# Performance work log

Hardware: AMD Instinct MI355X
Metric: run time of the kernel (lower is better)

The kernel has to match this reference:

```python
import jax, jax.numpy as jnp
from jax import lax
import numpy as np

NHEADS = 8

def _conv_block2d(x, w, b):
    y = lax.conv_general_dilated(x, w, (2, 2), [(1, 1), (1, 1)],
                                 dimension_numbers=('NCHW', 'OIHW', 'NCHW'))
    return jax.nn.gelu(y + b[None, :, None, None])

def _conv_block3d(x, w, b):
    y = lax.conv_general_dilated(x, w, (2, 2, 2), [(1, 1)] * 3,
                                 dimension_numbers=('NCDHW', 'OIDHW', 'NCDHW'))
    return jax.nn.gelu(y + b[None, :, None, None, None])

def _layernorm(x, g, b, eps=1e-5):
    mu = x.mean(-1, keepdims=True)
    var = x.var(-1, keepdims=True)
    return (x - mu) / jnp.sqrt(var + eps) * g + b

def _neighborhood_attn(x, g, bln, qkv_w, qkv_b, proj_w, proj_b, dw=5, hw=7, ww=7):
    # x: [B, C, D, H, W]; 3D neighborhood attention, window (dw,hw,ww), zero-pad + mask
    B, C, D, H, W = x.shape
    h, hd = NHEADS, C // NHEADS
    xt = jnp.transpose(x, (0, 2, 3, 4, 1))               # [B,D,H,W,C]
    y = _layernorm(xt, g, bln)
    qkv = y @ qkv_w + qkv_b                               # [B,D,H,W,3C]
    qkv = qkv.reshape(B, D, H, W, 3, h, hd)
    qkv = jnp.transpose(qkv, (4, 0, 5, 6, 1, 2, 3))       # [3,B,h,hd,D,H,W]
    q, k, v = qkv[0] * (hd ** -0.5), qkv[1], qkv[2]
    pz, py, px = dw // 2, hw // 2, ww // 2
    pad = ((0, 0), (0, 0), (0, 0), (pz, pz), (py, py), (px, px))
    kp, vp = jnp.pad(k, pad), jnp.pad(v, pad)
    valid = jnp.pad(jnp.ones((D, H, W), x.dtype), ((pz, pz), (py, py), (px, px)))
    offs = jnp.stack(jnp.meshgrid(jnp.arange(dw), jnp.arange(hw), jnp.arange(ww), indexing='ij'), -1).reshape(-1, 3)

    def score_step(_, o):
        ks = lax.dynamic_slice(kp, (0, 0, 0, o[0], o[1], o[2]), (B, h, hd, D, H, W))
        m = lax.dynamic_slice(valid, (o[0], o[1], o[2]), (D, H, W))
        return None, ((q * ks).sum(2), m)

    _, (scores, masks) = lax.scan(score_step, None, offs)  # [245,B,h,D,H,W],[245,D,H,W]
    neg = jnp.finfo(scores.dtype).min
    scores = jnp.where(masks[:, None, None] > 0, scores, neg)
    probs = jax.nn.softmax(scores, axis=0)

    def out_step(acc, xs):
        o, p = xs
        vs = lax.dynamic_slice(vp, (0, 0, 0, o[0], o[1], o[2]), (B, h, hd, D, H, W))
        return acc + p[:, :, None] * vs, None

    out0 = jnp.zeros((B, h, hd, D, H, W), x.dtype)
    out, _ = lax.scan(out_step, out0, (offs, probs))
    out = jnp.transpose(out, (0, 3, 4, 5, 1, 2)).reshape(B, D, H, W, C)
    out = out @ proj_w + proj_b
    return x + jnp.transpose(out, (0, 4, 1, 2, 3))

def setup_inputs() -> dict:
    key = jax.random.key(0)
    ks = jax.random.split(key, 16)
    rn = lambda i, shp, s: jax.random.normal(ks[i], shp, jnp.float32) * s
    return {
        'x_2d': rn(0, (1, 8, 256, 512), 1.0),
        'x_3d': rn(1, (1, 5, 24, 256, 512), 1.0),
        'sw0': rn(2, (128, 8, 3, 3), 0.02), 'sb0': jnp.zeros((128,), jnp.float32),
        'sw1': rn(3, (256, 128, 3, 3), 0.02), 'sb1': jnp.zeros((256,), jnp.float32),
        'sw2': rn(4, (512, 256, 3, 3), 0.02), 'sb2': jnp.zeros((512,), jnp.float32),
        'pw0': rn(5, (128, 5, 3, 3, 3), 0.02), 'pb0': jnp.zeros((128,), jnp.float32),
        'pw1': rn(6, (256, 128, 3, 3, 3), 0.02), 'pb1': jnp.zeros((256,), jnp.float32),
        'pw2': rn(7, (512, 256, 3, 3, 3), 0.02), 'pb2': jnp.zeros((512,), jnp.float32),
        'lat_w': rn(8, (512, 512, 1, 1, 1), 0.02), 'lat_b': jnp.zeros((512,), jnp.float32),
        'ln_g': jnp.ones((3, 512), jnp.float32), 'ln_b': jnp.zeros((3, 512), jnp.float32),
        'qkv_w': rn(9, (3, 512, 1536), 0.02), 'qkv_b': jnp.zeros((3, 1536), jnp.float32),
        'proj_w': rn(10, (3, 512, 512), 0.02), 'proj_b': jnp.zeros((3, 512), jnp.float32),
    }

def reference(x_2d, x_3d, sw0, sb0, sw1, sb1, sw2, sb2,
              pw0, pb0, pw1, pb1, pw2, pb2, lat_w, lat_b,
              ln_g, ln_b, qkv_w, qkv_b, proj_w, proj_b):
    s = x_2d
    for w_, b_ in ((sw0, sb0), (sw1, sb1), (sw2, sb2)):
        s = _conv_block2d(s, w_, b_)
    p = x_3d
    for w_, b_ in ((pw0, pb0), (pw1, pb1), (pw2, pb2)):
        p = _conv_block3d(p, w_, b_)
    feats = jnp.concatenate([p, s[:, :, None]], axis=2)   # [B,512,D/8+1,H/8,W/8]
    lat = lax.conv_general_dilated(feats, lat_w, (1, 1, 1), 'VALID',
                                   dimension_numbers=('NCDHW', 'OIDHW', 'NCDHW'))
    lat = lat + lat_b[None, :, None, None, None]
    for i in range(3):
        lat = _neighborhood_attn(lat, ln_g[i], ln_b[i], qkv_w[i], qkv_b[i], proj_w[i], proj_b[i])
    return lat
```

## Files before the change

kernel.cpp:

```cpp
#include <hip/hip_runtime.h>
#include <hip/hip_bf16.h>
#include <math.h>

typedef __hip_bfloat16 bf16;
typedef __attribute__((ext_vector_type(8))) short s8v;
typedef __attribute__((ext_vector_type(4))) float f4v;

__device__ __forceinline__ float ldf(const float* p) { return *p; }
__device__ __forceinline__ float ldf(const bf16* p) { return __bfloat162float(*p); }
__device__ __forceinline__ void stf(float* p, float v) { *p = v; }
__device__ __forceinline__ void stf(bf16* p, float v) { *p = __float2bfloat16(v); }

__device__ __forceinline__ float gelu_tanh(float x) {
    float x3 = x * x * x;
    return 0.5f * x * (1.f + tanhf(0.7978845608028654f * (x + 0.044715f * x3)));
}
__device__ __forceinline__ unsigned short bfbits(float x) {
    bf16 t = __float2bfloat16(x);
    return *(unsigned short*)&t;
}

__device__ __forceinline__ void gload16(const bf16* g, bf16* l)
{
    __builtin_amdgcn_global_load_lds(
        (const __attribute__((address_space(1))) unsigned int*)g,
        (__attribute__((address_space(3))) unsigned int*)l,
        16, 0, 0);
}

__global__ __launch_bounds__(256) void fill0_k(uint4* __restrict__ p, int n16)
{
    int i = blockIdx.x * 256 + threadIdx.x;
    if (i < n16) p[i] = uint4{0u, 0u, 0u, 0u};
}

__global__ __launch_bounds__(256) void wprep_k(const float* __restrict__ w, bf16* __restrict__ wr,
                                               int OC, int IC, int T)
{
    int i = blockIdx.x * 256 + threadIdx.x;
    if (i >= OC * IC * T) return;
    int t = i % T; int rem = i / T; int ic = rem % IC; int oc = rem / IC;
    wr[((size_t)t * OC + oc) * IC + ic] = __float2bfloat16(w[i]);
}

__global__ __launch_bounds__(256) void w1prep_k(const float* __restrict__ w, bf16* __restrict__ o,
                                                int OC, int nic, int ntap, int Kp)
{
    int i = blockIdx.x * 256 + threadIdx.x;
    if (i >= OC * Kp) return;
    int oc = i / Kp, k = i - oc * Kp;
    float v = 0.f;
    if (k < nic * ntap) {
        int tap = k / nic, ic = k - tap * nic;
        v = w[((size_t)oc * nic + ic) * ntap + tap];
    }
    o[i] = __float2bfloat16(v);
}

__global__ __launch_bounds__(256) void tprep_k(const float* __restrict__ w, bf16* __restrict__ wt,
                                               int K, int N)
{
    int i = blockIdx.x * 256 + threadIdx.x;
    if (i >= K * N) return;
    int n = i % N, k = i / N;
    wt[(size_t)n * K + k] = __float2bfloat16(w[i]);
}

__global__ __launch_bounds__(256) void cast_k(const float* __restrict__ w, bf16* __restrict__ o, int n)
{
    int i = blockIdx.x * 256 + threadIdx.x;
    if (i < n) o[i] = __float2bfloat16(w[i]);
}

__global__ __launch_bounds__(256) void im2col3d_k(const float* __restrict__ x, bf16* __restrict__ A, int od0)
{
    int gid = blockIdx.x * 256 + threadIdx.x;
    int m = gid / 20, kg = gid - 20 * (gid / 20);
    int ow = m & 255, rowid = m >> 8;
    int oh = rowid & 127, od = od0 + (rowid >> 7);
    int iz0 = 2 * od - 1, iy0 = 2 * oh - 1, ix0 = 2 * ow - 1;
    union { uint4 u; unsigned short h[8]; } pk;
#pragma unroll
    for (int j = 0; j < 8; j++) {
        int k = kg * 8 + j;
        float v = 0.f;
        if (k < 135) {
            int tap = k / 5, ic = k - tap * 5;
            int kz = tap / 9, r = tap - kz * 9;
            int ky = r / 3, kx = r - ky * 3;
            int iz = iz0 + kz, iy = iy0 + ky, ix = ix0 + kx;
            if ((unsigned)iz < 24u && (unsigned)iy < 256u && (unsigned)ix < 512u)
                v = x[(((size_t)ic * 24 + iz) * 256 + iy) * 512 + ix];
        }
        pk.h[j] = bfbits(v);
    }
    *(uint4*)&A[(size_t)m * 160 + kg * 8] = pk.u;
}

__global__ __launch_bounds__(256) void im2col2d_k(const float* __restrict__ x, bf16* __restrict__ A)
{
    int gid = blockIdx.x * 256 + threadIdx.x;
    int m = gid / 12, kg = gid - 12 * (gid / 12);
    int ow = m & 255, oh = m >> 8;
    int iy0 = 2 * oh - 1, ix0 = 2 * ow - 1;
    union { uint4 u; unsigned short h[8]; } pk;
#pragma unroll
    for (int j = 0; j < 8; j++) {
        int k = kg * 8 + j;
        float v = 0.f;
        if (k < 72) {
            int tap = k >> 3, ic = k & 7;
            int ky = tap / 3, kx = tap - ky * 3;
            int iy = iy0 + ky, ix = ix0 + kx;
            if ((unsigned)iy < 256u && (unsigned)ix < 512u)
                v = x[((size_t)ic * 256 + iy) * 512 + ix];
        }
        pk.h[j] = bfbits(v);
    }
    *(uint4*)&A[(size_t)m * 96 + kg * 8] = pk.u;
}

__global__ __launch_bounds__(256) void conv1_gemm(
    const bf16* __restrict__ A, const bf16* __restrict__ W, const float* __restrict__ bias,
    bf16* __restrict__ out, int M, int Kp, int rowOff)
{
    __shared__ __align__(16) bf16 As[128 * 32];
    __shared__ __align__(16) bf16 Bs[128 * 32];
    int tid = threadIdx.x;
    int m0 = blockIdx.x * 128;
    int wave = tid >> 6, lane = tid & 63;
    int wb = tid & 192;
    int wm = (wave >> 1) * 64, wn = (wave & 1) * 64;
    int lm = lane & 15, lq = lane >> 4;
    f4v acc[4][4];
#pragma unroll
    for (int i = 0; i < 4; i++)
#pragma unroll
        for (int j = 0; j < 4; j++) acc[i][j] = f4v{0.f, 0.f, 0.f, 0.f};
    for (int k0 = 0; k0 < Kp; k0 += 32) {
        __syncthreads();
#pragma unroll
        for (int c = 0; c < 2; c++) {
            int i = c * 256 + tid;
            int row = i >> 2, kq = i & 3;
            gload16(&A[(size_t)(m0 + row) * Kp + k0 + kq * 8], &As[(c * 256 + wb) * 8]);
            gload16(&W[(size_t)row * Kp + k0 + kq * 8], &Bs[(c * 256 + wb) * 8]);
        }
        __syncthreads();
        s8v af[4], bfr[4];
#pragma unroll
        for (int mi = 0; mi < 4; mi++) af[mi] = *(const s8v*)&As[(wm + mi * 16 + lm) * 32 + lq * 8];
#pragma unroll
        for (int ni = 0; ni < 4; ni++) bfr[ni] = *(const s8v*)&Bs[(wn + ni * 16 + lm) * 32 + lq * 8];
#pragma unroll
        for (int mi = 0; mi < 4; mi++)
#pragma unroll
            for (int ni = 0; ni < 4; ni++)
                acc[mi][ni] = __builtin_amdgcn_mfma_f32_16x16x32_bf16(af[mi], bfr[ni], acc[mi][ni], 0, 0, 0);
    }
#pragma unroll
    for (int mi = 0; mi < 4; mi++)
#pragma unroll
        for (int ni = 0; ni < 4; ni++)
#pragma unroll
            for (int r = 0; r < 4; r++) {
                int m = m0 + wm + mi * 16 + lq * 4 + r;
                int n = wn + ni * 16 + lm;
                int row = rowOff + (m >> 8), x = m & 255;
                float v = acc[mi][ni][r] + bias[n];
                out[((size_t)row * 258 + 1 + x) * 128 + n] = __float2bfloat16(gelu_tanh(v));
            }
}

template <int BM, int KD>
__global__ __launch_bounds__(256) void conv_mfma2(
    const bf16* __restrict__ in, const bf16* __restrict__ wr, const float* __restrict__ bias,
    bf16* __restrict__ out, int ID, int IH, int IWp, int IC,
    int OH, int OC, int OWS, int outPad, int nx)
{
    constexpr int NI = (BM == 128) ? 4 : 2;
    __shared__ __align__(16) bf16 As[3 * BM * 32];
    __shared__ __align__(16) bf16 Bs[3 * 128 * 32];
    int tid = threadIdx.x;
    int nwg = gridDim.x;
    int bl = blockIdx.x;
    int swz = (bl & 7) * (nwg >> 3) + (bl >> 3);
    int n0 = (swz % nx) * 128;
    int rowid = swz / nx;
    int od = rowid / OH, oh = rowid % OH;
    int wave = tid >> 6, lane = tid & 63;
    int wb = tid & 192;
    int wm = (BM == 128) ? (wave >> 1) * 64 : 0;
    int wn = (BM == 128) ? (wave & 1) * 64 : wave * 32;
    int lm = lane & 15, lq = lane >> 4;
    f4v acc[4][NI];
#pragma unroll
    for (int i = 0; i < 4; i++)
#pragma unroll
        for (int j = 0; j < NI; j++) acc[i][j] = f4v{0.f, 0.f, 0.f, 0.f};

    for (int kz = 0; kz < KD; kz++) {
        int iz = (KD == 3) ? (2 * od + kz - 1) : 0;
        if ((unsigned)iz >= (unsigned)ID) continue;
        for (int ky = 0; ky < 3; ky++) {
            int iy = 2 * oh + ky - 1;
            if ((unsigned)iy >= (unsigned)IH) continue;
            const bf16* inrow = in + ((size_t)iz * IH + iy) * IWp * IC;
            const bf16* wbase = wr + (size_t)((kz * 3 + ky) * 3) * OC * IC;
            for (int kb = 0; kb < IC; kb += 32) {
                __syncthreads();
#pragma unroll
                for (int c = 0; c < (3 * BM) / 64; c++) {
                    int i = c * 256 + tid;
                    int kx = i / (BM * 4);
                    int r = i - kx * (BM * 4);
                    int m = r >> 2, sub = r & 3;
                    gload16(&inrow[(size_t)(2 * m + kx) * IC + kb + sub * 8],
                            &As[(c * 256 + wb) * 8]);
                }
#pragma unroll
                for (int c = 0; c < 6; c++) {
                    int i = c * 256 + tid;
                    int t3 = i >> 9, r = i & 511, n = r >> 2, sub = r & 3;
                    gload16(&wbase[((size_t)t3 * OC + n0 + n) * IC + kb + sub * 8],
                            &Bs[(c * 256 + wb) * 8]);
                }
                __syncthreads();
#pragma unroll
                for (int kx = 0; kx < 3; kx++) {
                    s8v af[4], bfr[NI];
#pragma unroll
                    for (int mi = 0; mi < 4; mi++)
                        af[mi] = *(const s8v*)&As[(kx * BM + wm + mi * 16 + lm) * 32 + lq * 8];
#pragma unroll
                    for (int ni = 0; ni < NI; ni++)
                        bfr[ni] = *(const s8v*)&Bs[(kx * 128 + wn + ni * 16 + lm) * 32 + lq * 8];
#pragma unroll
                    for (int mi = 0; mi < 4; mi++)
#pragma unroll
                        for (int ni = 0; ni < NI; ni++)
                            acc[mi][ni] = __builtin_amdgcn_mfma_f32_16x16x32_bf16(af[mi], bfr[ni], acc[mi][ni], 0, 0, 0);
                }
            }
        }
    }
    size_t orowbase = ((size_t)rowid * OWS + outPad) * OC;
#pragma unroll
    for (int mi = 0; mi < 4; mi++)
#pragma unroll
        for (int ni = 0; ni < NI; ni++)
#pragma unroll
            for (int r = 0; r < 4; r++) {
                int m = wm + mi * 16 + lq * 4 + r;
                int n = n0 + wn + ni * 16 + lm;
                float v = acc[mi][ni][r] + bias[n];
                out[orowbase + (size_t)m * OC + n] = __float2bfloat16(gelu_tanh(v));
            }
}

template <typename OutT, int RES, int VT>
__global__ __launch_bounds__(256) void gemm_bt(
    const bf16* __restrict__ A, const bf16* __restrict__ Bt, const float* __restrict__ bias,
    OutT* __restrict__ C, const float* __restrict__ res, bf16* __restrict__ vt,
    int M, int N, int K)
{
    __shared__ __align__(16) bf16 As[128 * 32];
    __shared__ __align__(16) bf16 Bs[128 * 32];
    int tid = threadIdx.x;
    int n0 = blockIdx.x * 128, m0 = blockIdx.y * 128;
    int wave = tid >> 6, lane = tid & 63;
    int wb = tid & 192;
    int wm = (wave >> 1) * 64, wn = (wave & 1) * 64;
    int lm = lane & 15, lq = lane >> 4;
    f4v acc[4][4];
#pragma unroll
    for (int i = 0; i < 4; i++)
#pragma unroll
        for (int j = 0; j < 4; j++) acc[i][j] = f4v{0.f, 0.f, 0.f, 0.f};
    for (int k0 = 0; k0 < K; k0 += 32) {
        __syncthreads();
#pragma unroll
        for (int c = 0; c < 2; c++) {
            int i = c * 256 + tid;
            int row = i >> 2, kq = i & 3;
            gload16(&A[(size_t)(m0 + row) * K + k0 + kq * 8], &As[(c * 256 + wb) * 8]);
            gload16(&Bt[(size_t)(n0 + row) * K + k0 + kq * 8], &Bs[(c * 256 + wb) * 8]);
        }
        __syncthreads();
        s8v af[4], bfr[4];
#pragma unroll
        for (int mi = 0; mi < 4; mi++) af[mi] = *(const s8v*)&As[(wm + mi * 16 + lm) * 32 + lq * 8];
#pragma unroll
        for (int ni = 0; ni < 4; ni++) bfr[ni] = *(const s8v*)&Bs[(wn + ni * 16 + lm) * 32 + lq * 8];
#pragma unroll
        for (int mi = 0; mi < 4; mi++)
#pragma unroll
            for (int ni = 0; ni < 4; ni++)
                acc[mi][ni] = __builtin_amdgcn_mfma_f32_16x16x32_bf16(af[mi], bfr[ni], acc[mi][ni], 0, 0, 0);
    }
#pragma unroll
    for (int mi = 0; mi < 4; mi++)
#pragma unroll
        for (int ni = 0; ni < 4; ni++) {
            int n = n0 + wn + ni * 16 + lm;
            int mbase = m0 + wm + mi * 16 + lq * 4;
            float b = bias[n];
            if (VT && n >= 1024) {
                ushort4 pk;
                pk.x = bfbits(acc[mi][ni][0] + b);
                pk.y = bfbits(acc[mi][ni][1] + b);
                pk.z = bfbits(acc[mi][ni][2] + b);
                pk.w = bfbits(acc[mi][ni][3] + b);
                *(ushort4*)&vt[(size_t)(n - 1024) * 8192 + mbase] = pk;
            }
#pragma unroll
            for (int r = 0; r < 4; r++) {
                int m = mbase + r;
                float v = acc[mi][ni][r] + b;
                if (RES) v += res[(size_t)m * N + n];
                stf(&C[(size_t)m * N + n], v);
            }
        }
}

__global__ __launch_bounds__(256) void ln_k(
    const float* __restrict__ lat, const float* __restrict__ g, const float* __restrict__ b,
    bf16* __restrict__ y)
{
    int tok = blockIdx.x * 4 + (threadIdx.x >> 6);
    int lane = threadIdx.x & 63;
    const float4* row = (const float4*)&lat[(size_t)tok * 512 + lane * 8];
    float4 a = row[0], c = row[1];
    float s = a.x + a.y + a.z + a.w + c.x + c.y + c.z + c.w;
    float ss = a.x * a.x + a.y * a.y + a.z * a.z + a.w * a.w
             + c.x * c.x + c.y * c.y + c.z * c.z + c.w * c.w;
#pragma unroll
    for (int off = 32; off; off >>= 1) {
        s += __shfl_xor(s, off);
        ss += __shfl_xor(ss, off);
    }
    float mu = s * (1.f / 512.f);
    float var = ss * (1.f / 512.f) - mu * mu;
    float rstd = rsqrtf(var + 1e-5f);
    const float4* gp = (const float4*)&g[lane * 8];
    const float4* bp = (const float4*)&b[lane * 8];
    float4 g0 = gp[0], g1 = gp[1], b0 = bp[0], b1 = bp[1];
    union { uint4 u; unsigned short h[8]; } pk;
    pk.h[0] = bfbits((a.x - mu) * rstd * g0.x + b0.x);
    pk.h[1] = bfbits((a.y - mu) * rstd * g0.y + b0.y);
    pk.h[2] = bfbits((a.z - mu) * rstd * g0.z + b0.z);
    pk.h[3] = bfbits((a.w - mu) * rstd * g0.w + b0.w);
    pk.h[4] = bfbits((c.x - mu) * rstd * g1.x + b1.x);
    pk.h[5] = bfbits((c.y - mu) * rstd * g1.y + b1.y);
    pk.h[6] = bfbits((c.z - mu) * rstd * g1.z + b1.z);
    pk.h[7] = bfbits((c.w - mu) * rstd * g1.w + b1.w);
    *(uint4*)&y[(size_t)tok * 512 + lane * 8] = pk.u;
}

__global__ __launch_bounds__(256) void natt_mfma(
    const bf16* __restrict__ qkv, const bf16* __restrict__ vT, bf16* __restrict__ o)
{
    __shared__ __align__(16) char smem[46080];
    bf16* qs = (bf16*)smem;
    float* obuf = (float*)(smem + 11264);
    float* mlb = (float*)(smem + 44032);
    int tid = threadIdx.x;
    int bx = blockIdx.x;
    int rd = bx >> 5, rh = bx & 31;
    int d = (rd == 0) ? 1 : (rd == 1) ? 2 : (rd == 2) ? 0 : 3;
    int h = (rh < 26) ? (rh + 3) : (rh == 26) ? 2 : (rh == 27) ? 29
          : (rh == 28) ? 1 : (rh == 29) ? 30 : (rh == 30) ? 0 : 31;
    int rowid = d * 32 + h;
    int head = blockIdx.y;
    int rowbase = rowid * 64;
    int hoff = head * 64;
    int wave = tid >> 6, lane = tid & 63;
    int lm = lane & 15, lq = lane >> 4;
    bf16* pb = (bf16*)(smem + 11264 + wave * 8192);

    for (int i = tid; i < 512; i += 256) {
        int row = i >> 3, sub = i & 7;
        *(uint4*)&qs[row * 88 + sub * 8] =
            *(const uint4*)&qkv[(size_t)(rowbase + row) * 1536 + hoff + sub * 8];
    }
    {
        uint4 z{0u, 0u, 0u, 0u};
#pragma unroll
        for (int i = 0; i < 8; i++) ((uint4*)pb)[lane + i * 64] = z;
    }
    __syncthreads();

    f4v Oa[4][4];
#pragma unroll
    for (int i = 0; i < 4; i++)
#pragma unroll
        for (int j = 0; j < 4; j++) Oa[i][j] = f4v{0.f, 0.f, 0.f, 0.f};
    float mr[4][4], lr[4][4];
#pragma unroll
    for (int i = 0; i < 4; i++)
#pragma unroll
        for (int j = 0; j < 4; j++) { mr[i][j] = -1e30f; lr[i][j] = 0.f; }

    for (int idx = wave; idx < 35; idx += 4) {
        int dz = idx / 7 - 2, dy = idx % 7 - 3;
        int zz = d + dz, yy = h + dy;
        if ((unsigned)zz >= 4u || (unsigned)yy >= 32u) continue;
        int kbase = (zz * 32 + yy) * 64;
        s8v kf[4][2];
#pragma unroll
        for (int ni = 0; ni < 4; ni++)
#pragma unroll
            for (int c = 0; c < 2; c++)
                kf[ni][c] = *(const s8v*)&qkv[(size_t)(kbase + ni * 16 + lm) * 1536 + 512 + hoff + c * 32 + lq * 8];
#pragma unroll
        for (int mi = 0; mi < 4; mi++) {
            s8v qfc[2];
            qfc[0] = *(const s8v*)&qs[(mi * 16 + lm) * 88 + lq * 8];
            qfc[1] = *(const s8v*)&qs[(mi * 16 + lm) * 88 + 32 + lq * 8];
            f4v s[4];
#pragma unroll
            for (int ni = 0; ni < 4; ni++) s[ni] = f4v{0.f, 0.f, 0.f, 0.f};
            __builtin_amdgcn_s_setprio(1);
#pragma unroll
            for (int c = 0; c < 2; c++)
#pragma unroll
                for (int ni = 0; ni < 4; ni++)
                    s[ni] = __builtin_amdgcn_mfma_f32_16x16x32_bf16(qfc[c], kf[ni][c], s[ni], 0, 0, 0);
            __builtin_amdgcn_s_setprio(0);
#pragma unroll
            for (int r = 0; r < 4; r++) {
                int w0 = mi * 16 + lq * 4 + r;
                float s0v = s[0][r], s1v = s[1][r], s2v = s[2][r], s3v = s[3][r];
                int t = w0 + 8 - lm;
                int niq = (t < 0) ? 0 : (t >> 4);
                niq = (niq > 3) ? 3 : niq;
                float vlo = (niq & 1) ? s1v : s0v;
                float vhi = (niq & 1) ? s3v : s2v;
                float v = (niq & 2) ? vhi : vlo;
                int col = (niq << 4) | lm;
                int dlt = col - w0;
                float vv = ((unsigned)(dlt + 3) <= 6u) ? v * 0.125f : -1e30f;
                float rm = vv;
#pragma unroll
                for (int off = 1; off <= 8; off <<= 1)
                    rm = fmaxf(rm, __shfl_xor(rm, off));
                float mo = mr[mi][r];
                float mn = mo;
                if (__any(rm > mo)) {
                    mn = fmaxf(mo, rm);
                    float al = __expf(mo - mn);
                    mr[mi][r] = mn;
                    lr[mi][r] *= al;
#pragma unroll
                    for (int nd = 0; nd < 4; nd++)
                        Oa[mi][nd][r] *= al;
                }
                float p = __expf(vv - mn);
                float rs = p;
#pragma unroll
                for (int off = 1; off <= 8; off <<= 1)
                    rs += __shfl_xor(rs, off);
                lr[mi][r] += rs;
                pb[(w0 << 6) + (col ^ ((w0 & 7) << 3))] = __float2bfloat16(p);
            }
        }
        s8v vf[4][2];
#pragma unroll
        for (int nd = 0; nd < 4; nd++)
#pragma unroll
            for (int c = 0; c < 2; c++)
                vf[nd][c] = *(const s8v*)&vT[(size_t)(hoff + nd * 16 + lm) * 8192 + kbase + c * 32 + lq * 8];
        __asm__ __volatile__("s_waitcnt lgkmcnt(0)" ::: "memory");
        __builtin_amdgcn_sched_barrier(0);
#pragma unroll
        for (int c = 0; c < 2; c++) {
            s8v pf[4];
#pragma unroll
            for (int mi = 0; mi < 4; mi++)
                pf[mi] = *(const s8v*)&pb[((mi * 16 + lm) << 6) + ((c * 32 + lq * 8) ^ ((lm & 7) << 3))];
            __builtin_amdgcn_s_setprio(1);
#pragma unroll
            for (int mi = 0; mi < 4; mi++)
#pragma unroll
                for (int nd = 0; nd < 4; nd++)
                    Oa[mi][nd] = __builtin_amdgcn_mfma_f32_16x16x32_bf16(pf[mi], vf[nd][c], Oa[mi][nd], 0, 0, 0);
            __builtin_amdgcn_s_setprio(0);
        }
    }
    if (lm == 0) {
#pragma unroll
        for (int mi = 0; mi < 4; mi++)
#pragma unroll
            for (int r = 0; r < 4; r++) {
                int row = mi * 16 + lq * 4 + r;
                mlb[wave * 128 + row] = mr[mi][r];
                mlb[wave * 128 + 64 + row] = lr[mi][r];
            }
    }
    __syncthreads();
    for (int wv = 0; wv < 4; wv++) {
        if (wave == wv) {
#pragma unroll
            for (int mi = 0; mi < 4; mi++)
#pragma unroll
                for (int r = 0; r < 4; r++) {
                    int row = mi * 16 + lq * 4 + r;
                    float M = fmaxf(fmaxf(mlb[row], mlb[128 + row]),
                                    fmaxf(mlb[256 + row], mlb[384 + row]));
                    float sc = __expf(mr[mi][r] - M);
#pragma unroll
                    for (int nd = 0; nd < 4; nd++) {
                        int ci = row * 65 + nd * 16 + lm;
                        float add = Oa[mi][nd][r] * sc;
                        obuf[ci] = (wv == 0) ? add : (obuf[ci] + add);
                    }
                }
        }
        __syncthreads();
    }
    {
        int row = tid >> 2, cb = (tid & 3) * 16;
        float m0 = mlb[row], m1 = mlb[128 + row], m2 = mlb[256 + row], m3 = mlb[384 + row];
        float M = fmaxf(fmaxf(m0, m1), fmaxf(m2, m3));
        float L = mlb[64 + row] * __expf(m0 - M) + mlb[192 + row] * __expf(m1 - M)
                + mlb[320 + row] * __expf(m2 - M) + mlb[448 + row] * __expf(m3 - M);
        float inv = 1.f / L;
        union { uint4 u[2]; unsigned short hs[16]; } pk;
#pragma unroll
        for (int j = 0; j < 16; j++)
            pk.hs[j] = bfbits(obuf[row * 65 + cb + j] * inv);
        *(uint4*)&o[(size_t)(rowbase + row) * 512 + hoff + cb] = pk.u[0];
        *(uint4*)&o[(size_t)(rowbase + row) * 512 + hoff + cb + 8] = pk.u[1];
    }
}

__global__ __launch_bounds__(256) void tout_k(const float* __restrict__ lat, float* __restrict__ out)
{
    __shared__ float t[64][65];
    int p0 = blockIdx.x * 64, c0 = blockIdx.y * 64;
    for (int i = threadIdx.x; i < 4096; i += 256) {
        int r = i >> 6, cc = i & 63;
        t[r][cc] = lat[(size_t)(p0 + r) * 512 + c0 + cc];
    }
    __syncthreads();
    for (int i = threadIdx.x; i < 4096; i += 256) {
        int cc = i >> 6, r = i & 63;
        out[(size_t)(c0 + cc) * 8192 + p0 + r] = t[r][cc];
    }
}

extern "C" void kernel_launch(void* const* d_in, const int* in_sizes, int n_in,
                              void* d_out, int out_size, void* d_ws, size_t ws_size,
                              hipStream_t stream)
{
    const float* x2d = (const float*)d_in[0];
    const float* x3d = (const float*)d_in[1];
    const float* sw0 = (const float*)d_in[2];
    const float* sb0 = (const float*)d_in[3];
    const float* sw1 = (const float*)d_in[4];
    const float* sb1 = (const float*)d_in[5];
    const float* sw2 = (const float*)d_in[6];
    const float* sb2 = (const float*)d_in[7];
    const float* pw0 = (const float*)d_in[8];
    const float* pb0 = (const float*)d_in[9];
    const float* pw1 = (const float*)d_in[10];
    const float* pb1 = (const float*)d_in[11];
    const float* pw2 = (const float*)d_in[12];
    const float* pb2 = (const float*)d_in[13];
    const float* latw = (const float*)d_in[14];
    const float* latb = (const float*)d_in[15];
    const float* lng = (const float*)d_in[16];
    const float* lnb = (const float*)d_in[17];
    const float* qkvw = (const float*)d_in[18];
    const float* qkvb = (const float*)d_in[19];
    const float* projw = (const float*)d_in[20];
    const float* projb = (const float*)d_in[21];
    float* outp = (float*)d_out;

    char* ws = (char*)d_ws;
    bf16* p0pad = (bf16*)(ws + 0);
    bf16* wr3d2 = (bf16*)(ws + 101449728ull);
    bf16* wr3d3 = (bf16*)(ws + 103219200ull);
    bf16* wr2d2 = (bf16*)(ws + 110297088ull);
    bf16* wr2d3 = (bf16*)(ws + 110886912ull);
    bf16* qkvt  = (bf16*)(ws + 113246208ull);
    bf16* projt = (bf16*)(ws + 117964800ull);
    bf16* latbf = (bf16*)(ws + 119537664ull);
    bf16* w13d  = (bf16*)(ws + 120061952ull);
    bf16* w12d  = (bf16*)(ws + 120102912ull);
    bf16* p1pad = (bf16*)(ws + 120127488ull);
    bf16* s0pad = (bf16*)(ws + 145686528ull);
    bf16* s1pad = (bf16*)(ws + 154140672ull);
    bf16* featsT= (bf16*)(ws + 158400512ull);
    float* lat  = (float*)(ws + 166789120ull);
    bf16* A3 = (bf16*)(ws + 120127488ull);
    bf16* A2 = (bf16*)(ws + 158400512ull);
    bf16* ybf    = (bf16*)(ws + 0);
    bf16* qkvbuf = (bf16*)(ws + 8388608ull);
    bf16* attno  = (bf16*)(ws + 33554432ull);
    bf16* vT     = (bf16*)(ws + 41943040ull);

    wprep_k<<<3456, 256, 0, stream>>>(pw1, wr3d2, 256, 128, 27);
    wprep_k<<<13824, 256, 0, stream>>>(pw2, wr3d3, 512, 256, 27);
    wprep_k<<<1152, 256, 0, stream>>>(sw1, wr2d2, 256, 128, 9);
    wprep_k<<<4608, 256, 0, stream>>>(sw2, wr2d3, 512, 256, 9);
    for (int r = 0; r < 3; r++) {
        tprep_k<<<3072, 256, 0, stream>>>(qkvw + (size_t)r * 786432, qkvt + (size_t)r * 786432, 512, 1536);
        tprep_k<<<1024, 256, 0, stream>>>(projw + (size_t)r * 262144, projt + (size_t)r * 262144, 512, 512);
    }
    cast_k<<<1024, 256, 0, stream>>>(latw, latbf, 262144);
    w1prep_k<<<80, 256, 0, stream>>>(pw0, w13d, 128, 5, 27, 160);
    w1prep_k<<<48, 256, 0, stream>>>(sw0, w12d, 128, 8, 9, 96);

    fill0_k<<<24768, 256, 0, stream>>>((uint4*)p0pad, 6340608);

    im2col3d_k<<<15360, 256, 0, stream>>>(x3d, A3, 0);
    conv1_gemm<<<1536, 256, 0, stream>>>(A3, w13d, pb0, p0pad, 196608, 160, 0);
    im2col3d_k<<<15360, 256, 0, stream>>>(x3d, A3, 6);
    conv1_gemm<<<1536, 256, 0, stream>>>(A3, w13d, pb0, p0pad, 196608, 160, 768);

    fill0_k<<<9344, 256, 0, stream>>>((uint4*)p1pad, 2392064);
    im2col2d_k<<<1536, 256, 0, stream>>>(x2d, A2);
    conv1_gemm<<<256, 256, 0, stream>>>(A2, w12d, sb0, s0pad, 32768, 96, 0);

    conv_mfma2<128, 1><<<dim3(128), 256, 0, stream>>>(s0pad, wr2d2, sb1, s1pad, 1, 128, 258, 128, 64, 256, 130, 1, 2);
    conv_mfma2<64, 1><<<dim3(128), 256, 0, stream>>>(s1pad, wr2d3, sb2, featsT + (size_t)6144 * 512, 1, 64, 130, 256, 32, 512, 64, 0, 4);
    conv_mfma2<128, 3><<<dim3(768), 256, 0, stream>>>(p0pad, wr3d2, pb1, p1pad, 12, 128, 258, 128, 64, 256, 130, 1, 2);
    conv_mfma2<64, 3><<<dim3(384), 256, 0, stream>>>(p1pad, wr3d3, pb2, featsT, 6, 64, 130, 256, 32, 512, 64, 0, 4);

    gemm_bt<float, 0, 0><<<dim3(4, 64), 256, 0, stream>>>(featsT, latbf, latb, lat, nullptr, nullptr, 8192, 512, 512);

    for (int r = 0; r < 3; r++) {
        ln_k<<<2048, 256, 0, stream>>>(lat, lng + r * 512, lnb + r * 512, ybf);
        gemm_bt<bf16, 0, 1><<<dim3(12, 64), 256, 0, stream>>>(ybf, qkvt + (size_t)r * 786432, qkvb + r * 1536,
                                                              qkvbuf, nullptr, vT, 8192, 1536, 512);
        natt_mfma<<<dim3(128, 8), 256, 0, stream>>>(qkvbuf, vT, attno);
        gemm_bt<float, 1, 0><<<dim3(4, 64), 256, 0, stream>>>(attno, projt + (size_t)r * 262144, projb + r * 512,
                                                              lat, lat, nullptr, 8192, 512, 512);
    }

    tout_k<<<dim3(128, 8), 256, 0, stream>>>(lat, outp);
}
```

Measured before the change: 1.391 ms.

## Split attention query rows across two wave groups with 512-thread blocks

The neighborhood-attention kernel now runs 8 waves per block instead of 4. Each pair of waves shares a key/value slab offset, and each wave handles half of the 64 query rows, so per-wave accumulator registers are halved and more waves hide latency. The shared Q tile moves to an XOR-swizzled layout with no padding, and shared memory shrinks by overlapping Q storage with the softmax stat buffer; an extra barrier guards that reuse. In exchange, K and V fragments are loaded twice from global memory per slab (once by each half), and the merge epilogue has more threads.

Measured after the change: 1.213 ms. 1.15x faster.

```diff
diff --git a/kernel.cpp b/kernel.cpp
--- a/kernel.cpp
+++ b/kernel.cpp
@@ -357,13 +357,12 @@
     *(uint4*)&y[(size_t)tok * 512 + lane * 8] = pk.u;
 }
 
-__global__ __launch_bounds__(256) void natt_mfma(
+__global__ __launch_bounds__(512) void natt_mfma(
     const bf16* __restrict__ qkv, const bf16* __restrict__ vT, bf16* __restrict__ o)
 {
-    __shared__ __align__(16) char smem[46080];
-    bf16* qs = (bf16*)smem;
-    float* obuf = (float*)(smem + 11264);
-    float* mlb = (float*)(smem + 44032);
+    __shared__ __align__(16) char smem[40960];
+    float* mlb = (float*)smem;
+    float* obuf = (float*)(smem + 8192);
     int tid = threadIdx.x;
     int bx = blockIdx.x;
     int rd = bx >> 5, rh = bx & 31;
@@ -375,33 +374,35 @@
     int rowbase = rowid * 64;
     int hoff = head * 64;
     int wave = tid >> 6, lane = tid & 63;
+    int olane = wave & 3, rhalf = wave >> 2;
     int lm = lane & 15, lq = lane >> 4;
-    bf16* pb = (bf16*)(smem + 11264 + wave * 8192);
-
-    for (int i = tid; i < 512; i += 256) {
-        int row = i >> 3, sub = i & 7;
-        *(uint4*)&qs[row * 88 + sub * 8] =
+    char* qsb = smem;
+    bf16* pb = (bf16*)(smem + 8192 + olane * 8192);
+
+    {
+        int row = tid >> 3, sub = tid & 7;
+        *(uint4*)(qsb + row * 128 + ((sub * 16) ^ ((row & 7) << 4))) =
             *(const uint4*)&qkv[(size_t)(rowbase + row) * 1536 + hoff + sub * 8];
     }
     {
         uint4 z{0u, 0u, 0u, 0u};
-#pragma unroll
-        for (int i = 0; i < 8; i++) ((uint4*)pb)[lane + i * 64] = z;
+        uint4* zp = (uint4*)(smem + 8192);
+        zp[tid] = z; zp[tid + 512] = z; zp[tid + 1024] = z; zp[tid + 1536] = z;
     }
     __syncthreads();
 
-    f4v Oa[4][4];
-#pragma unroll
-    for (int i = 0; i < 4; i++)
+    f4v Oa[2][4];
+#pragma unroll
+    for (int i = 0; i < 2; i++)
 #pragma unroll
         for (int j = 0; j < 4; j++) Oa[i][j] = f4v{0.f, 0.f, 0.f, 0.f};
-    float mr[4][4], lr[4][4];
-#pragma unroll
-    for (int i = 0; i < 4; i++)
+    float mr[2][4], lr[2][4];
+#pragma unroll
+    for (int i = 0; i < 2; i++)
 #pragma unroll
         for (int j = 0; j < 4; j++) { mr[i][j] = -1e30f; lr[i][j] = 0.f; }
 
-    for (int idx = wave; idx < 35; idx += 4) {
+    for (int idx = olane; idx < 35; idx += 4) {
         int dz = idx / 7 - 2, dy = idx % 7 - 3;
         int zz = d + dz, yy = h + dy;
         if ((unsigned)zz >= 4u || (unsigned)yy >= 32u) continue;
@@ -413,19 +414,21 @@
             for (int c = 0; c < 2; c++)
                 kf[ni][c] = *(const s8v*)&qkv[(size_t)(kbase + ni * 16 + lm) * 1536 + 512 + hoff + c * 32 + lq * 8];
 #pragma unroll
-        for (int mi = 0; mi < 4; mi++) {
-            s8v qfc[2];
-            qfc[0] = *(const s8v*)&qs[(mi * 16 + lm) * 88 + lq * 8];
-            qfc[1] = *(const s8v*)&qs[(mi * 16 + lm) * 88 + 32 + lq * 8];
+        for (int mj = 0; mj < 2; mj++) {
+            int mi = rhalf * 2 + mj;
+            int qrow = mi * 16 + lm;
+            s8v qc0 = *(const s8v*)(qsb + qrow * 128 + ((lq * 16) ^ ((qrow & 7) << 4)));
+            s8v qc1 = *(const s8v*)(qsb + qrow * 128 + ((64 + lq * 16) ^ ((qrow & 7) << 4)));
             f4v s[4];
 #pragma unroll
             for (int ni = 0; ni < 4; ni++) s[ni] = f4v{0.f, 0.f, 0.f, 0.f};
             __builtin_amdgcn_s_setprio(1);
 #pragma unroll
-            for (int c = 0; c < 2; c++)
-#pragma unroll
-                for (int ni = 0; ni < 4; ni++)
-                    s[ni] = __builtin_amdgcn_mfma_f32_16x16x32_bf16(qfc[c], kf[ni][c], s[ni], 0, 0, 0);
+            for (int ni = 0; ni < 4; ni++)
+                s[ni] = __builtin_amdgcn_mfma_f32_16x16x32_bf16(qc0, kf[ni][0], s[ni], 0, 0, 0);
+#pragma unroll
+            for (int ni = 0; ni < 4; ni++)
+                s[ni] = __builtin_amdgcn_mfma_f32_16x16x32_bf16(qc1, kf[ni][1], s[ni], 0, 0, 0);
             __builtin_amdgcn_s_setprio(0);
 #pragma unroll
             for (int r = 0; r < 4; r++) {
@@ -444,23 +447,23 @@
 #pragma unroll
                 for (int off = 1; off <= 8; off <<= 1)
                     rm = fmaxf(rm, __shfl_xor(rm, off));
-                float mo = mr[mi][r];
+                float mo = mr[mj][r];
                 float mn = mo;
                 if (__any(rm > mo)) {
                     mn = fmaxf(mo, rm);
                     float al = __expf(mo - mn);
-                    mr[mi][r] = mn;
-                    lr[mi][r] *= al;
+                    mr[mj][r] = mn;
+                    lr[mj][r] *= al;
 #pragma unroll
                     for (int nd = 0; nd < 4; nd++)
-                        Oa[mi][nd][r] *= al;
+                        Oa[mj][nd][r] *= al;
                 }
                 float p = __expf(vv - mn);
                 float rs = p;
 #pragma unroll
                 for (int off = 1; off <= 8; off <<= 1)
                     rs += __shfl_xor(rs, off);
-                lr[mi][r] += rs;
+                lr[mj][r] += rs;
                 pb[(w0 << 6) + (col ^ ((w0 & 7) << 3))] = __float2bfloat16(p);
             }
         }
@@ -474,44 +477,47 @@
         __builtin_amdgcn_sched_barrier(0);
 #pragma unroll
         for (int c = 0; c < 2; c++) {
-            s8v pf[4];
-#pragma unroll
-            for (int mi = 0; mi < 4; mi++)
-                pf[mi] = *(const s8v*)&pb[((mi * 16 + lm) << 6) + ((c * 32 + lq * 8) ^ ((lm & 7) << 3))];
+            s8v pf[2];
+#pragma unroll
+            for (int mj = 0; mj < 2; mj++) {
+                int mi = rhalf * 2 + mj;
+                pf[mj] = *(const s8v*)&pb[((mi * 16 + lm) << 6) + ((c * 32 + lq * 8) ^ ((lm & 7) << 3))];
+            }
             __builtin_amdgcn_s_setprio(1);
 #pragma unroll
-            for (int mi = 0; mi < 4; mi++)
+            for (int mj = 0; mj < 2; mj++)
 #pragma unroll
                 for (int nd = 0; nd < 4; nd++)
-                    Oa[mi][nd] = __builtin_amdgcn_mfma_f32_16x16x32_bf16(pf[mi], vf[nd][c], Oa[mi][nd], 0, 0, 0);
+                    Oa[mj][nd] = __builtin_amdgcn_mfma_f32_16x16x32_bf16(pf[mj], vf[nd][c], Oa[mj][nd], 0, 0, 0);
             __builtin_amdgcn_s_setprio(0);
         }
     }
+    __syncthreads();
     if (lm == 0) {
 #pragma unroll
-        for (int mi = 0; mi < 4; mi++)
+        for (int mj = 0; mj < 2; mj++)
 #pragma unroll
             for (int r = 0; r < 4; r++) {
-                int row = mi * 16 + lq * 4 + r;
-                mlb[wave * 128 + row] = mr[mi][r];
-                mlb[wave * 128 + 64 + row] = lr[mi][r];
+                int row = (rhalf * 2 + mj) * 16 + lq * 4 + r;
+                mlb[olane * 128 + row] = mr[mj][r];
+                mlb[olane * 128 + 64 + row] = lr[mj][r];
             }
     }
     __syncthreads();
     for (int wv = 0; wv < 4; wv++) {
-        if (wave == wv) {
-#pragma unroll
-            for (int mi = 0; mi < 4; mi++)
+        if (olane == wv) {
+#pragma unroll
+            for (int mj = 0; mj < 2; mj++)
 #pragma unroll
                 for (int r = 0; r < 4; r++) {
-                    int row = mi * 16 + lq * 4 + r;
+                    int row = (rhalf * 2 + mj) * 16 + lq * 4 + r;
                     float M = fmaxf(fmaxf(mlb[row], mlb[128 + row]),
                                     fmaxf(mlb[256 + row], mlb[384 + row]));
-                    float sc = __expf(mr[mi][r] - M);
+                    float sc = __expf(mr[mj][r] - M);
 #pragma unroll
                     for (int nd = 0; nd < 4; nd++) {
                         int ci = row * 65 + nd * 16 + lm;
-                        float add = Oa[mi][nd][r] * sc;
+                        float add = Oa[mj][nd][r] * sc;
                         obuf[ci] = (wv == 0) ? add : (obuf[ci] + add);
                     }
                 }
@@ -519,18 +525,17 @@
         __syncthreads();
     }
     {
-        int row = tid >> 2, cb = (tid & 3) * 16;
+        int row = tid >> 3, cb = (tid & 7) * 8;
         float m0 = mlb[row], m1 = mlb[128 + row], m2 = mlb[256 + row], m3 = mlb[384 + row];
         float M = fmaxf(fmaxf(m0, m1), fmaxf(m2, m3));
         float L = mlb[64 + row] * __expf(m0 - M) + mlb[192 + row] * __expf(m1 - M)
                 + mlb[320 + row] * __expf(m2 - M) + mlb[448 + row] * __expf(m3 - M);
         float inv = 1.f / L;
-        union { uint4 u[2]; unsigned short hs[16]; } pk;
-#pragma unroll
-        for (int j = 0; j < 16; j++)
+        union { uint4 u; unsigned short hs[8]; } pk;
+#pragma unroll
+        for (int j = 0; j < 8; j++)
             pk.hs[j] = bfbits(obuf[row * 65 + cb + j] * inv);
-        *(uint4*)&o[(size_t)(rowbase + row) * 512 + hoff + cb] = pk.u[0];
-        *(uint4*)&o[(size_t)(rowbase + row) * 512 + hoff + cb + 8] = pk.u[1];
+        *(uint4*)&o[(size_t)(rowbase + row) * 512 + hoff + cb] = pk.u;
     }
 }
 
@@ -634,7 +639,7 @@
         ln_k<<<2048, 256, 0, stream>>>(lat, lng + r * 512, lnb + r * 512, ybf);
         gemm_bt<bf16, 0, 1><<<dim3(12, 64), 256, 0, stream>>>(ybf, qkvt + (size_t)r * 786432, qkvb + r * 1536,
                                                               qkvbuf, nullptr, vT, 8192, 1536, 512);
-        natt_mfma<<<dim3(128, 8), 256, 0, stream>>>(qkvbuf, vT, attno);
+        natt_mfma<<<dim3(128, 8), 512, 0, stream>>>(qkvbuf, vT, attno);
         gemm_bt<float, 1, 0><<<dim3(4, 64), 256, 0, stream>>>(attno, projt + (size_t)r * 262144, projb + r * 512,
                                                               lat, lat, nullptr, 8192, 512, 512);
     }
```
